# Performance work log

Measured on AMD Instinct MI355X. Metric: run time of the kernel, lower is better.

## Reference

```python
import jax, jax.numpy as jnp
import numpy as np

FEATURE_WEIGHTS = {"local": 0.4, "phrase": 0.4, "global": 0.2, "input": 0.1}
ADV_WEIGHTS = (0.4, 0.4, 0.2)  # stage_2 progressive weights
NOTE_OFF_START = 128
TIME_SHIFT_START = 256
VELOCITY_START = 768
EPS = 1e-12


def setup_inputs() -> dict:
    key = jax.random.key(0)
    ks = jax.random.split(key, 12)
    B, S, P, D = 32, 2048, 128, 512
    f = lambda k, shp: jax.random.normal(k, shp, dtype=jnp.float32)
    return {
        "real_local": f(ks[0], (B, S, D)),
        "real_phrase": f(ks[1], (B, P, D)),
        "real_global": f(ks[2], (B, D)),
        "real_input": f(ks[3], (B, S, D)),
        "fake_local": f(ks[4], (B, S, D)),
        "fake_phrase": f(ks[5], (B, P, D)),
        "fake_global": f(ks[6], (B, D)),
        "fake_input": f(ks[7], (B, S, D)),
        "local_logits": f(ks[8], (B, S)),
        "phrase_logits": f(ks[9], (B, P)),
        "global_logits": f(ks[10], (B, 1)),
        "tokens": jax.random.randint(ks[11], (B, S), 0, 774, dtype=jnp.int32),
    }


def _l2_normalize(x):
    # matches F.normalize(p=2, dim=-1): x / max(||x||, eps)
    n = jnp.sqrt(jnp.sum(x * x, axis=-1, keepdims=True))
    return x / jnp.maximum(n, EPS)


def _feature_matching(real_feats, fake_feats):
    total = 0.0
    for name, w in FEATURE_WEIGHTS.items():
        r = _l2_normalize(real_feats[name])
        f = _l2_normalize(fake_feats[name])
        diff = f.mean(axis=0) - jax.lax.stop_gradient(r.mean(axis=0))
        total = total + w * jnp.mean(diff * diff)
    return total / len(FEATURE_WEIGHTS)


def _musical_perceptual(tokens):
    B, S = tokens.shape
    # rhythm consistency
    time_shifts = ((tokens >= TIME_SHIFT_START) & (tokens < VELOCITY_START)).astype(jnp.float32)
    rhythm = jnp.mean(jnp.abs(jnp.diff(time_shifts, axis=1)))
    # harmonic coherence (vectorized form of the per-timestep python loop:
    # sum over i of batch-mean, then divide by seq_len)
    note_on = tokens < NOTE_OFF_START
    pitches = tokens * note_on.astype(tokens.dtype)
    pc = pitches % 12
    interval = jnp.abs(pc[:, :-1] - pc[:, 1:])
    harsh = ((interval == 6) | (interval == 11)).astype(jnp.float32)
    harmony = jnp.sum(jnp.mean(harsh, axis=0)) / S
    # melodic smoothness
    pdiff = jnp.diff(pitches.astype(jnp.float32), axis=1)
    melody = jnp.mean((jnp.abs(pdiff) > 12).astype(jnp.float32))
    return rhythm + harmony + melody


def _bce_with_logits_ones(logits):
    # BCEWithLogits(x, target=1) = softplus(-x)
    return jnp.mean(jax.nn.softplus(-logits))


def _adversarial(local_logits, phrase_logits, global_logits):
    w = ADV_WEIGHTS
    return (w[0] * _bce_with_logits_ones(local_logits)
            + w[1] * _bce_with_logits_ones(phrase_logits)
            + w[2] * _bce_with_logits_ones(global_logits))


def reference(real_local, real_phrase, real_global, real_input,
              fake_local, fake_phrase, fake_global, fake_input,
              local_logits, phrase_logits, global_logits, tokens):
    real_feats = {"local": real_local, "phrase": real_phrase,
                  "global": real_global, "input": real_input}
    fake_feats = {"local": fake_local, "phrase": fake_phrase,
                  "global": fake_global, "input": fake_input}
    fm = _feature_matching(real_feats, fake_feats)
    musical = _musical_perceptual(tokens)
    adv = _adversarial(local_logits, phrase_logits, global_logits)
    return fm + musical + adv
```

## Files before the change

### kernel.cpp

```cpp
#include <hip/hip_runtime.h>
#include <math.h>


#define B_ 32
#define S_ 2048
#define P_ 128
#define D_ 512

#define TILE_S 4
#define NT_LOCAL  (S_ / TILE_S)
#define NT_INPUT  (S_ / TILE_S)
#define NT_PHRASE (P_ / TILE_S)
#define NTASK (NT_LOCAL + NT_INPUT + NT_PHRASE + 1)

__global__ void zero_out_kernel(float* out) {
    if (threadIdx.x == 0 && blockIdx.x == 0) out[0] = 0.0f;
}

__device__ __forceinline__ float sum8(float4 a, float4 b) {
    return a.x * a.x + a.y * a.y + a.z * a.z + a.w * a.w
         + b.x * b.x + b.y * b.y + b.z * b.z + b.w * b.w;
}

__global__ __launch_bounds__(256) void fm_stream(
    const float* __restrict__ real_local, const float* __restrict__ real_phrase,
    const float* __restrict__ real_global, const float* __restrict__ real_input,
    const float* __restrict__ fake_local, const float* __restrict__ fake_phrase,
    const float* __restrict__ fake_global, const float* __restrict__ fake_input,
    float* __restrict__ out)
{
    const int task = blockIdx.x;
    const int w = threadIdx.x >> 6;
    const int c = threadIdx.x & 63;

    const float* rp; const float* fp;
    long long rowBase;
    long long rs4;
    float scale;
    bool active = true;

    if (task < NT_LOCAL) {
        rp = real_local; fp = fake_local;
        rowBase = (long long)(task * TILE_S + w) * D_;
        rs4 = (long long)S_ * D_ / 4;
        scale = 0.4f / (4.0f * 1024.0f * (float)S_ * (float)D_);
    } else if (task < NT_LOCAL + NT_INPUT) {
        int t = task - NT_LOCAL;
        rp = real_input; fp = fake_input;
        rowBase = (long long)(t * TILE_S + w) * D_;
        rs4 = (long long)S_ * D_ / 4;
        scale = 0.1f / (4.0f * 1024.0f * (float)S_ * (float)D_);
    } else if (task < NT_LOCAL + NT_INPUT + NT_PHRASE) {
        int t = task - NT_LOCAL - NT_INPUT;
        rp = real_phrase; fp = fake_phrase;
        rowBase = (long long)(t * TILE_S + w) * D_;
        rs4 = (long long)P_ * D_ / 4;
        scale = 0.4f / (4.0f * 1024.0f * (float)P_ * (float)D_);
    } else {
        rp = real_global; fp = fake_global;
        rowBase = 0;
        rs4 = D_ / 4;
        scale = 0.2f / (4.0f * 1024.0f * (float)D_);
        active = (w == 0);
    }

    float4 a0 = make_float4(0.f, 0.f, 0.f, 0.f);
    float4 a1 = make_float4(0.f, 0.f, 0.f, 0.f);

    if (active) {
        const float4* r4 = (const float4*)(rp + rowBase);
        const float4* f4 = (const float4*)(fp + rowBase);
        #pragma unroll 2
        for (int b = 0; b < B_; ++b) {
            const float4* rb = r4 + (long long)b * rs4;
            const float4* fb = f4 + (long long)b * rs4;
            float4 x0 = rb[c];
            float4 x1 = rb[64 + c];
            float4 y0 = fb[c];
            float4 y1 = fb[64 + c];

            float ssr = sum8(x0, x1);
            float ssf = sum8(y0, y1);
            #pragma unroll
            for (int off = 1; off <= 32; off <<= 1) {
                ssr += __shfl_xor(ssr, off, 64);
                ssf += __shfl_xor(ssf, off, 64);
            }
            float ir = -1.0f / fmaxf(sqrtf(ssr), 1e-12f);
            float jf =  1.0f / fmaxf(sqrtf(ssf), 1e-12f);

            a0.x = fmaf(x0.x, ir, fmaf(y0.x, jf, a0.x));
            a0.y = fmaf(x0.y, ir, fmaf(y0.y, jf, a0.y));
            a0.z = fmaf(x0.z, ir, fmaf(y0.z, jf, a0.z));
            a0.w = fmaf(x0.w, ir, fmaf(y0.w, jf, a0.w));
            a1.x = fmaf(x1.x, ir, fmaf(y1.x, jf, a1.x));
            a1.y = fmaf(x1.y, ir, fmaf(y1.y, jf, a1.y));
            a1.z = fmaf(x1.z, ir, fmaf(y1.z, jf, a1.z));
            a1.w = fmaf(x1.w, ir, fmaf(y1.w, jf, a1.w));
        }
    }

    float ssq = sum8(a0, a1);
    #pragma unroll
    for (int off = 1; off <= 32; off <<= 1)
        ssq += __shfl_xor(ssq, off, 64);

    __shared__ float wave_sums[4];
    if (c == 0) wave_sums[w] = ssq;
    __syncthreads();
    if (threadIdx.x == 0) {
        float t = wave_sums[0] + wave_sums[1] + wave_sums[2] + wave_sums[3];
        atomicAdd(out, t * scale);
    }
}

__device__ __forceinline__ float softplus_neg(float x) {
    float z = -x;
    return fmaxf(z, 0.0f) + log1pf(expf(-fabsf(z)));
}

__global__ __launch_bounds__(256) void small_kernel(
    const float* __restrict__ local_logits,
    const float* __restrict__ phrase_logits,
    const float* __restrict__ global_logits,
    const int* __restrict__ tokens,
    float* __restrict__ out)
{
    int gid = blockIdx.x * blockDim.x + threadIdx.x;
    float acc = 0.0f;

    const int NPAIR = B_ * (S_ - 1);
    if (gid < NPAIR) {
        int b = gid / (S_ - 1);
        int j = gid - b * (S_ - 1);
        int t0 = tokens[b * S_ + j];
        int t1 = tokens[b * S_ + j + 1];
        float ts0 = (t0 >= 256 && t0 < 768) ? 1.0f : 0.0f;
        float ts1 = (t1 >= 256 && t1 < 768) ? 1.0f : 0.0f;
        float rhythm = fabsf(ts1 - ts0);
        int p0 = (t0 < 128) ? t0 : 0;
        int p1 = (t1 < 128) ? t1 : 0;
        int iv = abs(p0 % 12 - p1 % 12);
        float harsh = (iv == 6 || iv == 11) ? 1.0f : 0.0f;
        float mel = (abs(p1 - p0) > 12) ? 1.0f : 0.0f;
        acc += rhythm * (1.0f / (float)NPAIR)
             + harsh * (1.0f / ((float)B_ * (float)S_))
             + mel * (1.0f / (float)NPAIR);
    }

    if (gid < B_ * S_)   acc += 0.4f * softplus_neg(local_logits[gid])  / (float)(B_ * S_);
    if (gid < B_ * P_)   acc += 0.4f * softplus_neg(phrase_logits[gid]) / (float)(B_ * P_);
    if (gid < B_)        acc += 0.2f * softplus_neg(global_logits[gid]) / (float)B_;

    #pragma unroll
    for (int off = 32; off > 0; off >>= 1)
        acc += __shfl_xor(acc, off, 64);

    __shared__ float warp_sums[4];
    int wid = threadIdx.x >> 6;
    int lane = threadIdx.x & 63;
    if (lane == 0) warp_sums[wid] = acc;
    __syncthreads();
    if (threadIdx.x == 0) {
        float t = warp_sums[0] + warp_sums[1] + warp_sums[2] + warp_sums[3];
        atomicAdd(out, t);
    }
}

extern "C" void kernel_launch(void* const* d_in, const int* in_sizes, int n_in,
                              void* d_out, int out_size, void* d_ws, size_t ws_size,
                              hipStream_t stream) {
    const float* real_local   = (const float*)d_in[0];
    const float* real_phrase  = (const float*)d_in[1];
    const float* real_global  = (const float*)d_in[2];
    const float* real_input   = (const float*)d_in[3];
    const float* fake_local   = (const float*)d_in[4];
    const float* fake_phrase  = (const float*)d_in[5];
    const float* fake_global  = (const float*)d_in[6];
    const float* fake_input   = (const float*)d_in[7];
    const float* local_logits  = (const float*)d_in[8];
    const float* phrase_logits = (const float*)d_in[9];
    const float* global_logits = (const float*)d_in[10];
    const int*   tokens        = (const int*)d_in[11];
    float* out = (float*)d_out;

    zero_out_kernel<<<1, 64, 0, stream>>>(out);

    fm_stream<<<NTASK, 256, 0, stream>>>(
        real_local, real_phrase, real_global, real_input,
        fake_local, fake_phrase, fake_global, fake_input, out);

    small_kernel<<<(B_ * S_) / 256, 256, 0, stream>>>(
        local_logits, phrase_logits, global_logits, tokens, out);
}
```

Measured before the change: 463.7 us.

## Split batch across waves per row and software-prefetch next batch row

Each block now handles one feature row (one s index) instead of four. Its four waves split the 32-batch reduction, eight batches each, and combine their per-column accumulators through shared memory before the final squared-norm reduction. The loop is fully unrolled with explicit prefetch of the next batch's loads, and launch bounds request higher occupancy. This raises block count and memory-level parallelism and shortens each wave's serial chain, at the cost of more atomics and more shared-memory traffic.

```diff
diff --git a/kernel.cpp b/kernel.cpp
--- a/kernel.cpp
+++ b/kernel.cpp
@@ -7,11 +7,12 @@
 #define P_ 128
 #define D_ 512
 
-#define TILE_S 4
-#define NT_LOCAL  (S_ / TILE_S)
-#define NT_INPUT  (S_ / TILE_S)
-#define NT_PHRASE (P_ / TILE_S)
+#define NT_LOCAL  S_
+#define NT_INPUT  S_
+#define NT_PHRASE P_
 #define NTASK (NT_LOCAL + NT_INPUT + NT_PHRASE + 1)
+
+#define BPW (B_ / 4)
 
 __global__ void zero_out_kernel(float* out) {
     if (threadIdx.x == 0 && blockIdx.x == 0) out[0] = 0.0f;
@@ -22,7 +23,7 @@
          + b.x * b.x + b.y * b.y + b.z * b.z + b.w * b.w;
 }
 
-__global__ __launch_bounds__(256) void fm_stream(
+__global__ __launch_bounds__(256, 8) void fm_stream(
     const float* __restrict__ real_local, const float* __restrict__ real_phrase,
     const float* __restrict__ real_global, const float* __restrict__ real_input,
     const float* __restrict__ fake_local, const float* __restrict__ fake_phrase,
@@ -37,23 +38,22 @@
     long long rowBase;
     long long rs4;
     float scale;
-    bool active = true;
 
     if (task < NT_LOCAL) {
         rp = real_local; fp = fake_local;
-        rowBase = (long long)(task * TILE_S + w) * D_;
+        rowBase = (long long)task * D_;
         rs4 = (long long)S_ * D_ / 4;
         scale = 0.4f / (4.0f * 1024.0f * (float)S_ * (float)D_);
     } else if (task < NT_LOCAL + NT_INPUT) {
         int t = task - NT_LOCAL;
         rp = real_input; fp = fake_input;
-        rowBase = (long long)(t * TILE_S + w) * D_;
+        rowBase = (long long)t * D_;
         rs4 = (long long)S_ * D_ / 4;
         scale = 0.1f / (4.0f * 1024.0f * (float)S_ * (float)D_);
     } else if (task < NT_LOCAL + NT_INPUT + NT_PHRASE) {
         int t = task - NT_LOCAL - NT_INPUT;
         rp = real_phrase; fp = fake_phrase;
-        rowBase = (long long)(t * TILE_S + w) * D_;
+        rowBase = (long long)t * D_;
         rs4 = (long long)P_ * D_ / 4;
         scale = 0.4f / (4.0f * 1024.0f * (float)P_ * (float)D_);
     } else {
@@ -61,56 +61,70 @@
         rowBase = 0;
         rs4 = D_ / 4;
         scale = 0.2f / (4.0f * 1024.0f * (float)D_);
-        active = (w == 0);
-    }
+    }
+
+    const float4* rb = (const float4*)(rp + rowBase) + (long long)(w * BPW) * rs4;
+    const float4* fb = (const float4*)(fp + rowBase) + (long long)(w * BPW) * rs4;
 
     float4 a0 = make_float4(0.f, 0.f, 0.f, 0.f);
     float4 a1 = make_float4(0.f, 0.f, 0.f, 0.f);
 
-    if (active) {
-        const float4* r4 = (const float4*)(rp + rowBase);
-        const float4* f4 = (const float4*)(fp + rowBase);
-        #pragma unroll 2
-        for (int b = 0; b < B_; ++b) {
-            const float4* rb = r4 + (long long)b * rs4;
-            const float4* fb = f4 + (long long)b * rs4;
-            float4 x0 = rb[c];
-            float4 x1 = rb[64 + c];
-            float4 y0 = fb[c];
-            float4 y1 = fb[64 + c];
-
-            float ssr = sum8(x0, x1);
-            float ssf = sum8(y0, y1);
-            #pragma unroll
-            for (int off = 1; off <= 32; off <<= 1) {
-                ssr += __shfl_xor(ssr, off, 64);
-                ssf += __shfl_xor(ssf, off, 64);
-            }
-            float ir = -1.0f / fmaxf(sqrtf(ssr), 1e-12f);
-            float jf =  1.0f / fmaxf(sqrtf(ssf), 1e-12f);
-
-            a0.x = fmaf(x0.x, ir, fmaf(y0.x, jf, a0.x));
-            a0.y = fmaf(x0.y, ir, fmaf(y0.y, jf, a0.y));
-            a0.z = fmaf(x0.z, ir, fmaf(y0.z, jf, a0.z));
-            a0.w = fmaf(x0.w, ir, fmaf(y0.w, jf, a0.w));
-            a1.x = fmaf(x1.x, ir, fmaf(y1.x, jf, a1.x));
-            a1.y = fmaf(x1.y, ir, fmaf(y1.y, jf, a1.y));
-            a1.z = fmaf(x1.z, ir, fmaf(y1.z, jf, a1.z));
-            a1.w = fmaf(x1.w, ir, fmaf(y1.w, jf, a1.w));
+    float4 x0 = rb[c], x1 = rb[64 + c];
+    float4 y0 = fb[c], y1 = fb[64 + c];
+
+    #pragma unroll
+    for (int i = 0; i < BPW; ++i) {
+        float4 nx0 = x0, nx1 = x1, ny0 = y0, ny1 = y1;
+        if (i < BPW - 1) {
+            rb += rs4; fb += rs4;
+            nx0 = rb[c]; nx1 = rb[64 + c];
+            ny0 = fb[c]; ny1 = fb[64 + c];
         }
-    }
-
-    float ssq = sum8(a0, a1);
-    #pragma unroll
-    for (int off = 1; off <= 32; off <<= 1)
-        ssq += __shfl_xor(ssq, off, 64);
-
-    __shared__ float wave_sums[4];
-    if (c == 0) wave_sums[w] = ssq;
+
+        float ssr = sum8(x0, x1);
+        float ssf = sum8(y0, y1);
+        #pragma unroll
+        for (int off = 1; off <= 32; off <<= 1) {
+            ssr += __shfl_xor(ssr, off, 64);
+            ssf += __shfl_xor(ssf, off, 64);
+        }
+        float ir = -1.0f / fmaxf(sqrtf(ssr), 1e-12f);
+        float jf =  1.0f / fmaxf(sqrtf(ssf), 1e-12f);
+
+        a0.x = fmaf(x0.x, ir, fmaf(y0.x, jf, a0.x));
+        a0.y = fmaf(x0.y, ir, fmaf(y0.y, jf, a0.y));
+        a0.z = fmaf(x0.z, ir, fmaf(y0.z, jf, a0.z));
+        a0.w = fmaf(x0.w, ir, fmaf(y0.w, jf, a0.w));
+        a1.x = fmaf(x1.x, ir, fmaf(y1.x, jf, a1.x));
+        a1.y = fmaf(x1.y, ir, fmaf(y1.y, jf, a1.y));
+        a1.z = fmaf(x1.z, ir, fmaf(y1.z, jf, a1.z));
+        a1.w = fmaf(x1.w, ir, fmaf(y1.w, jf, a1.w));
+
+        x0 = nx0; x1 = nx1; y0 = ny0; y1 = ny1;
+    }
+
+    __shared__ float wacc[3][8][64];
+    if (w > 0) {
+        int wi = w - 1;
+        wacc[wi][0][c] = a0.x; wacc[wi][1][c] = a0.y;
+        wacc[wi][2][c] = a0.z; wacc[wi][3][c] = a0.w;
+        wacc[wi][4][c] = a1.x; wacc[wi][5][c] = a1.y;
+        wacc[wi][6][c] = a1.z; wacc[wi][7][c] = a1.w;
+    }
     __syncthreads();
-    if (threadIdx.x == 0) {
-        float t = wave_sums[0] + wave_sums[1] + wave_sums[2] + wave_sums[3];
-        atomicAdd(out, t * scale);
+    if (w == 0) {
+        #pragma unroll
+        for (int wi = 0; wi < 3; ++wi) {
+            a0.x += wacc[wi][0][c]; a0.y += wacc[wi][1][c];
+            a0.z += wacc[wi][2][c]; a0.w += wacc[wi][3][c];
+            a1.x += wacc[wi][4][c]; a1.y += wacc[wi][5][c];
+            a1.z += wacc[wi][6][c]; a1.w += wacc[wi][7][c];
+        }
+        float ssq = sum8(a0, a1);
+        #pragma unroll
+        for (int off = 1; off <= 32; off <<= 1)
+            ssq += __shfl_xor(ssq, off, 64);
+        if (c == 0) atomicAdd(out, ssq * scale);
     }
 }
 
```

After: 465.8 us. Within noise of the previous version (+0.4%).
